# Optimization experiments

Measured on AMD Instinct MI355X. Metric: run time of the kernel, lower is better.

## Reference

```python
import jax, jax.numpy as jnp
import numpy as np

B, T, D, FF, H, K = 8, 1024, 512, 2048, 8, 15
HD = D // H  # key_dim = d_model // num_heads


def _ln(x, g, b):
    # keras LayerNormalization default epsilon = 1e-3
    m = jnp.mean(x, axis=-1, keepdims=True)
    v = jnp.var(x, axis=-1, keepdims=True)
    return (x - m) * jax.lax.rsqrt(v + 1e-3) * g + b


def setup_inputs() -> dict:
    key = jax.random.key(0)
    ks = iter(jax.random.split(key, 64))

    def rn(shape, s=0.02):
        return jax.random.normal(next(ks), shape, jnp.float32) * s

    p = {}
    p['x'] = jax.random.normal(next(ks), (B, T, D), jnp.float32)
    # ff_pre: LN -> Dense(FF, relu) -> Dense(D)
    p['g1'] = jnp.ones((D,), jnp.float32); p['b1'] = jnp.zeros((D,), jnp.float32)
    p['Wff1'] = rn((D, FF)); p['bff1'] = jnp.zeros((FF,), jnp.float32)
    p['Wff2'] = rn((FF, D)); p['bff2'] = jnp.zeros((D,), jnp.float32)
    # attention norm + MHA projections (keras EinsumDense shapes)
    p['ga'] = jnp.ones((D,), jnp.float32); p['ba'] = jnp.zeros((D,), jnp.float32)
    p['Wq'] = rn((D, H, HD)); p['bq'] = jnp.zeros((H, HD), jnp.float32)
    p['Wk'] = rn((D, H, HD)); p['bk'] = jnp.zeros((H, HD), jnp.float32)
    p['Wv'] = rn((D, H, HD)); p['bv'] = jnp.zeros((H, HD), jnp.float32)
    p['Wo'] = rn((H, HD, D)); p['bo'] = jnp.zeros((D,), jnp.float32)
    # conv branch: LN -> pointwise conv (2D, gelu) -> depthwise conv(k=15) -> BN -> swish -> pointwise conv (D)
    p['gc'] = jnp.ones((D,), jnp.float32); p['bc'] = jnp.zeros((D,), jnp.float32)
    p['Wcp'] = rn((D, 2 * D)); p['bcp'] = jnp.zeros((2 * D,), jnp.float32)
    p['dwk'] = rn((K, 1, 2 * D)); p['dwb'] = jnp.zeros((2 * D,), jnp.float32)
    p['bn_g'] = jnp.ones((2 * D,), jnp.float32); p['bn_b'] = jnp.zeros((2 * D,), jnp.float32)
    p['bn_m'] = jnp.zeros((2 * D,), jnp.float32)
    p['bn_v'] = jnp.ones((2 * D,), jnp.float32)
    p['Wco'] = rn((2 * D, D)); p['bco'] = jnp.zeros((D,), jnp.float32)
    # ff_post
    p['g2'] = jnp.ones((D,), jnp.float32); p['b2'] = jnp.zeros((D,), jnp.float32)
    p['Wf1'] = rn((D, FF)); p['bf1'] = jnp.zeros((FF,), jnp.float32)
    p['Wf2'] = rn((FF, D)); p['bf2'] = jnp.zeros((D,), jnp.float32)
    return p


def reference(x, g1, b1, Wff1, bff1, Wff2, bff2, ga, ba, Wq, bq, Wk, bk, Wv, bv, Wo, bo, gc, bc, Wcp, bcp, dwk, dwb, bn_g, bn_b, bn_m, bn_v, Wco, bco, g2, b2, Wf1, bf1, Wf2, bf2):
    # Macaron FFN (pre), half-step residual applied later
    x_ff = jnp.maximum(_ln(x, g1, b1) @ Wff1 + bff1, 0.0) @ Wff2 + bff2

    # causal multi-head self-attention (cache=None path)
    a = _ln(x, ga, ba)
    q = jnp.einsum('btd,dhk->bthk', a, Wq) + bq
    k = jnp.einsum('btd,dhk->bthk', a, Wk) + bk
    v = jnp.einsum('btd,dhk->bthk', a, Wv) + bv
    scores = jnp.einsum('bqhd,bkhd->bhqk', q, k) / jnp.sqrt(jnp.float32(HD))
    causal = jnp.tril(jnp.ones((T, T), bool))  # [T,T]
    scores = jnp.where(causal, scores, jnp.float32(-1e9))
    w = jax.nn.softmax(scores, axis=-1)
    ctx = jnp.einsum('bhqk,bkhd->bqhd', w, v)
    attn = jnp.einsum('bqhd,hdo->bqo', ctx, Wo) + bo

    x = x + 0.5 * x_ff + attn

    # convolution module: pointwise(gelu) -> causal left-pad -> depthwise -> BN(inference) -> swish -> pointwise
    c = jax.nn.gelu(_ln(x, gc, bc) @ Wcp + bcp, approximate=False)
    c = jnp.pad(c, ((0, 0), (K - 1, 0), (0, 0)))  # causal pad
    c = jax.lax.conv_general_dilated(
        c, dwk, window_strides=(1,), padding='VALID',
        dimension_numbers=('NWC', 'WIO', 'NWC'), feature_group_count=2 * D) + dwb
    c = (c - bn_m) * jax.lax.rsqrt(bn_v + 1e-3) * bn_g + bn_b
    c = c * jax.nn.sigmoid(c)  # swish
    c = c @ Wco + bco
    x = x + c

    # post FFN (full residual)
    x = x + (jnp.maximum(_ln(x, g2, b2) @ Wf1 + bf1, 0.0) @ Wf2 + bf2)
    return x
```

## Files before the change

### kernel.cpp

```cpp
#include <hip/hip_runtime.h>
#include <hip/hip_bf16.h>
#include <math.h>

#define BB 8
#define TT 1024
#define DD 512
#define FFD 2048
#define HH 8
#define HDD 64
#define KW 15
#define MR (BB*TT)
#define QKVN 1536

typedef __attribute__((ext_vector_type(8))) short short8;
typedef __attribute__((ext_vector_type(4))) short short4v;
typedef __attribute__((ext_vector_type(4))) float f32x4;
typedef __hip_bfloat16 bf16;

__device__ __forceinline__ float bf2f(unsigned u16) {
    return __uint_as_float(u16 << 16);
}

__device__ __forceinline__ void async_copy16(const void* g, void* l) {
    __builtin_amdgcn_global_load_lds(
        (const __attribute__((address_space(1))) void*)g,
        (__attribute__((address_space(3))) void*)l, 16, 0, 0);
}

__device__ __forceinline__ float gelu_exact(float v) {
    return 0.5f * v * (1.0f + erff(v * 0.70710678118654752f));
}

struct PrepPack {
    const float* src[10];
    bf16*        dst[10];
    int          K[10];
    int          lgNT[10];
    float        scale[10];
    int          off[10];
    const float* bq; const float* bk; const float* bv;
    float*       bdst;
    const float* x;
    const float* g1; const float* b1; const float* ga; const float* ba;
    bf16* o1; bf16* o2;
};

__global__ __launch_bounds__(256) void prep_kernel(PrepPack P) {
    __shared__ alignas(16) bf16 T[64][72];
    const int bid = blockIdx.x;
    if (bid == 1536) {
        #pragma unroll
        for (int it = 0; it < 6; ++it) {
            int i = it * 256 + threadIdx.x;
            float v = i < 512 ? P.bq[i] * 0.125f
                              : (i < 1024 ? P.bk[i - 512] : P.bv[i - 1024]);
            P.bdst[i] = v;
        }
        return;
    }
    if (bid > 1536) {
        int wave = ((bid - 1537) * 256 + (int)threadIdx.x) >> 6;
        int lane = threadIdx.x & 63;
        const float* row = P.x + (size_t)wave * DD;
        float4 v0 = ((const float4*)row)[lane];
        float4 v1 = ((const float4*)row)[64 + lane];
        float s  = v0.x + v0.y + v0.z + v0.w + v1.x + v1.y + v1.z + v1.w;
        float ss = v0.x*v0.x + v0.y*v0.y + v0.z*v0.z + v0.w*v0.w
                 + v1.x*v1.x + v1.y*v1.y + v1.z*v1.z + v1.w*v1.w;
        #pragma unroll
        for (int off = 32; off >= 1; off >>= 1) {
            s  += __shfl_xor(s,  off, 64);
            ss += __shfl_xor(ss, off, 64);
        }
        float mean = s * (1.0f / DD);
        float var  = ss * (1.0f / DD) - mean * mean;
        float r    = rsqrtf(var + 1e-3f);
        float n0x = (v0.x - mean) * r, n0y = (v0.y - mean) * r,
              n0z = (v0.z - mean) * r, n0w = (v0.w - mean) * r;
        float n1x = (v1.x - mean) * r, n1y = (v1.y - mean) * r,
              n1z = (v1.z - mean) * r, n1w = (v1.w - mean) * r;
        {
            float4 g0 = ((const float4*)P.g1)[lane];
            float4 gg = ((const float4*)P.g1)[64 + lane];
            float4 b0 = ((const float4*)P.b1)[lane];
            float4 bb = ((const float4*)P.b1)[64 + lane];
            alignas(8) bf16 o0[4], o1[4];
            o0[0] = __float2bfloat16(n0x * g0.x + b0.x);
            o0[1] = __float2bfloat16(n0y * g0.y + b0.y);
            o0[2] = __float2bfloat16(n0z * g0.z + b0.z);
            o0[3] = __float2bfloat16(n0w * g0.w + b0.w);
            o1[0] = __float2bfloat16(n1x * gg.x + bb.x);
            o1[1] = __float2bfloat16(n1y * gg.y + bb.y);
            o1[2] = __float2bfloat16(n1z * gg.z + bb.z);
            o1[3] = __float2bfloat16(n1w * gg.w + bb.w);
            bf16* orow = P.o1 + (size_t)wave * DD;
            *(short4v*)(orow + lane * 4)       = *(const short4v*)o0;
            *(short4v*)(orow + 256 + lane * 4) = *(const short4v*)o1;
        }
        {
            float4 g0 = ((const float4*)P.ga)[lane];
            float4 gg = ((const float4*)P.ga)[64 + lane];
            float4 b0 = ((const float4*)P.ba)[lane];
            float4 bb = ((const float4*)P.ba)[64 + lane];
            alignas(8) bf16 o0[4], o1[4];
            o0[0] = __float2bfloat16(n0x * g0.x + b0.x);
            o0[1] = __float2bfloat16(n0y * g0.y + b0.y);
            o0[2] = __float2bfloat16(n0z * g0.z + b0.z);
            o0[3] = __float2bfloat16(n0w * g0.w + b0.w);
            o1[0] = __float2bfloat16(n1x * gg.x + bb.x);
            o1[1] = __float2bfloat16(n1y * gg.y + bb.y);
            o1[2] = __float2bfloat16(n1z * gg.z + bb.z);
            o1[3] = __float2bfloat16(n1w * gg.w + bb.w);
            bf16* orow = P.o2 + (size_t)wave * DD;
            *(short4v*)(orow + lane * 4)       = *(const short4v*)o0;
            *(short4v*)(orow + 256 + lane * 4) = *(const short4v*)o1;
        }
        return;
    }
    int e = 0;
    #pragma unroll
    for (int i = 1; i < 10; ++i) e = (bid >= P.off[i]) ? i : e;
    const float* W  = P.src[e];
    bf16*        Wt = P.dst[e];
    const int    K  = P.K[e];
    const int    lg = P.lgNT[e];
    const float  scale = P.scale[e];
    const int local = bid - P.off[e];
    const int bx = local & ((1 << lg) - 1);
    const int by = local >> lg;
    const int k0 = by * 64;
    const int n0 = bx * 64;
    const int N  = (1 << lg) * 64;
    const int tid = threadIdx.x;
    #pragma unroll
    for (int it = 0; it < 4; ++it) {
        int lin = it * 256 + tid;
        int kl  = lin >> 4;
        int nq  = (lin & 15) * 4;
        float4 v = *(const float4*)(W + (size_t)(k0 + kl) * N + n0 + nq);
        T[nq + 0][kl] = __float2bfloat16(v.x * scale);
        T[nq + 1][kl] = __float2bfloat16(v.y * scale);
        T[nq + 2][kl] = __float2bfloat16(v.z * scale);
        T[nq + 3][kl] = __float2bfloat16(v.w * scale);
    }
    __syncthreads();
    #pragma unroll
    for (int it = 0; it < 4; ++it) {
        int lin = it * 256 + tid;
        int nl  = lin >> 4;
        int kq  = (lin & 15) * 4;
        *(short4v*)(Wt + (size_t)(n0 + nl) * K + k0 + kq) = *(const short4v*)&T[nl][kq];
    }
}

__global__ __launch_bounds__(256) void ln_kernel(const float* __restrict__ x,
                                                 const float* __restrict__ g,
                                                 const float* __restrict__ b,
                                                 bf16* __restrict__ out) {
    int wave = (blockIdx.x * blockDim.x + threadIdx.x) >> 6;
    int lane = threadIdx.x & 63;
    if (wave >= MR) return;
    const float* row = x + (size_t)wave * DD;
    float4 v0 = ((const float4*)row)[lane];
    float4 v1 = ((const float4*)row)[64 + lane];
    float s  = v0.x + v0.y + v0.z + v0.w + v1.x + v1.y + v1.z + v1.w;
    float ss = v0.x*v0.x + v0.y*v0.y + v0.z*v0.z + v0.w*v0.w
             + v1.x*v1.x + v1.y*v1.y + v1.z*v1.z + v1.w*v1.w;
    #pragma unroll
    for (int off = 32; off >= 1; off >>= 1) {
        s  += __shfl_xor(s,  off, 64);
        ss += __shfl_xor(ss, off, 64);
    }
    float mean = s * (1.0f / DD);
    float var  = ss * (1.0f / DD) - mean * mean;
    float r    = rsqrtf(var + 1e-3f);
    float4 g0 = ((const float4*)g)[lane];
    float4 g1 = ((const float4*)g)[64 + lane];
    float4 b0 = ((const float4*)b)[lane];
    float4 b1 = ((const float4*)b)[64 + lane];
    alignas(8) bf16 o0[4], o1[4];
    o0[0] = __float2bfloat16((v0.x - mean) * r * g0.x + b0.x);
    o0[1] = __float2bfloat16((v0.y - mean) * r * g0.y + b0.y);
    o0[2] = __float2bfloat16((v0.z - mean) * r * g0.z + b0.z);
    o0[3] = __float2bfloat16((v0.w - mean) * r * g0.w + b0.w);
    o1[0] = __float2bfloat16((v1.x - mean) * r * g1.x + b1.x);
    o1[1] = __float2bfloat16((v1.y - mean) * r * g1.y + b1.y);
    o1[2] = __float2bfloat16((v1.z - mean) * r * g1.z + b1.z);
    o1[3] = __float2bfloat16((v1.w - mean) * r * g1.w + b1.w);
    bf16* orow = out + (size_t)wave * DD;
    *(short4v*)(orow + lane * 4)       = *(const short4v*)o0;
    *(short4v*)(orow + 256 + lane * 4) = *(const short4v*)o1;
}

template<int BN, int OP, int RESMODE, int OUTMODE>
__global__ __launch_bounds__(256) void bgemm_kernel(
    const bf16* __restrict__ A,
    const bf16* __restrict__ Bt,
    const float* __restrict__ bias,
    const float* __restrict__ res1,
    const bf16* __restrict__ res2,
    float s2, float oscale,
    void* __restrict__ Cout,
    int N, int Kd, int nxb)
{
    constexpr int NT = BN / 32;
    __shared__ alignas(16) bf16 As[128][64];
    __shared__ alignas(16) bf16 Bs[BN][64];
    const int tid  = threadIdx.x;
    const int w    = tid >> 6;
    const int lane = tid & 63;
    const int quad = lane >> 4;
    const int l16  = lane & 15;
    const int wm   = w >> 1, wn = w & 1;

    const int flat = blockIdx.x;
    const int c8   = flat & 7;
    const int j    = flat >> 3;
    const int jy   = j / nxb;
    const int m0   = (c8 * 8 + jy) * 128;
    const int n0   = (j - jy * nxb) * BN;

    const int srow = lane >> 3;
    const int scol = ((lane & 7) ^ srow) * 8;

    const bf16* Ap = A  + (size_t)(m0 + w * 32 + srow) * Kd + scol;
    const bf16* Bp = Bt + (size_t)(n0 + w * (BN / 4) + srow) * Kd + scol;

    f32x4 acc[4][NT] = {};

    for (int k0 = 0; k0 < Kd; k0 += 64) {
        #pragma unroll
        for (int i = 0; i < 4; ++i)
            async_copy16(Ap + (size_t)(i * 8) * Kd + k0, &As[w * 32 + i * 8][0]);
        #pragma unroll
        for (int i = 0; i < BN / 32; ++i)
            async_copy16(Bp + (size_t)(i * 8) * Kd + k0, &Bs[w * (BN / 4) + i * 8][0]);
        __syncthreads();
        #pragma unroll
        for (int ks = 0; ks < 2; ++ks) {
            short8 af[4], bfr[NT];
            #pragma unroll
            for (int mt = 0; mt < 4; ++mt) {
                const int row = wm * 64 + mt * 16 + l16;
                const int c   = ((ks * 4 + quad) ^ (row & 7)) * 16;
                af[mt] = *(const short8*)((const char*)&As[row][0] + c);
            }
            #pragma unroll
            for (int nt = 0; nt < NT; ++nt) {
                const int col = wn * (BN / 2) + nt * 16 + l16;
                const int c   = ((ks * 4 + quad) ^ (col & 7)) * 16;
                bfr[nt] = *(const short8*)((const char*)&Bs[col][0] + c);
            }
            #pragma unroll
            for (int mt = 0; mt < 4; ++mt)
                #pragma unroll
                for (int nt = 0; nt < NT; ++nt)
                    acc[mt][nt] = __builtin_amdgcn_mfma_f32_16x16x32_bf16(
                        af[mt], bfr[nt], acc[mt][nt], 0, 0, 0);
        }
        __syncthreads();
    }

    const int crow0 = m0 + wm * 64 + quad * 4;
    const int ccol0 = n0 + wn * (BN / 2) + l16;
    #pragma unroll
    for (int nt = 0; nt < NT; ++nt) {
        const int col = ccol0 + nt * 16;
        const float bv = bias[col];
        #pragma unroll
        for (int mt = 0; mt < 4; ++mt) {
            #pragma unroll
            for (int r = 0; r < 4; ++r) {
                const int row = crow0 + mt * 16 + r;
                const size_t off = (size_t)row * N + col;
                float o = acc[mt][nt][r] + bv;
                if (OP == 1)      o = fmaxf(o, 0.f);
                else if (OP == 2) o = gelu_exact(o);
                if (RESMODE >= 1) o += res1[off];
                if (RESMODE == 2) o += s2 * __bfloat162float(res2[off]);
                if (OUTMODE == 0) ((float*)Cout)[off] = o;
                else              ((bf16*)Cout)[off]  = __float2bfloat16(o * oscale);
            }
        }
    }
}

__global__ __launch_bounds__(512, 2) void gemm256_kernel(
    const bf16* __restrict__ Aff, const bf16* __restrict__ Btff,
    const float* __restrict__ biasff, bf16* __restrict__ outff,
    const bf16* __restrict__ Aqk, const bf16* __restrict__ Btqk,
    const float* __restrict__ biasqk, bf16* __restrict__ qkvb,
    bf16* __restrict__ Vtb, int nffblk)
{
    __shared__ alignas(16) char lds[131072];
    const int tid  = threadIdx.x;
    const int w    = tid >> 6;
    const int lane = tid & 63;
    const int quad = lane >> 4;
    const int l16  = lane & 15;
    const int wm   = w >> 2, wn = w & 3;

    const bool jobq = (int)blockIdx.x >= nffblk;
    const int  flat = jobq ? (int)blockIdx.x - nffblk : (int)blockIdx.x;
    const int  nxb  = jobq ? 6 : 8;
    const bf16* A   = jobq ? Aqk : Aff;
    const bf16* Bt  = jobq ? Btqk : Btff;
    const float* bias = jobq ? biasqk : biasff;

    const int c8 = flat & 7;
    const int j  = flat >> 3;
    const int jy = j / nxb;
    const int m0 = (c8 * 4 + jy) * 256;
    const int n0 = (j - jy * nxb) * 256;

    const bf16* ApS = A  + (size_t)(m0 + w * 32 + (lane >> 2)) * DD + (lane & 3) * 8;
    const bf16* BpS = Bt + (size_t)(n0 + w * 32 + (lane >> 2)) * DD + (lane & 3) * 8;
    char* ldsW = lds + w * 2048;

#define STAGE_A(kc, boff) do { \
        async_copy16(ApS + (kc),            ldsW + (boff));        \
        async_copy16(ApS + 16 * DD + (kc),  ldsW + (boff) + 1024); } while (0)
#define STAGE_B(kc, boff) do { \
        async_copy16(BpS + (kc),            ldsW + (boff));        \
        async_copy16(BpS + 16 * DD + (kc),  ldsW + (boff) + 1024); } while (0)

    const int aoff = (wm * 128 + l16) * 64 + quad * 16;
    const int boff = 32768 + (wn * 64 + l16) * 64 + quad * 16;

    f32x4 acc[8][4] = {};

#define CLUSTER(MH) \
    asm volatile("" ::: "memory"); \
    __builtin_amdgcn_s_barrier(); \
    asm volatile("s_waitcnt lgkmcnt(0)" ::: "memory"); \
    __builtin_amdgcn_sched_barrier(0); \
    __builtin_amdgcn_s_setprio(1); \
    _Pragma("unroll") \
    for (int mt = 0; mt < 4; ++mt) \
        _Pragma("unroll") \
        for (int nt = 0; nt < 4; ++nt) \
            acc[(MH) * 4 + mt][nt] = __builtin_amdgcn_mfma_f32_16x16x32_bf16( \
                af[mt], bf[nt], acc[(MH) * 4 + mt][nt], 0, 0, 0); \
    __builtin_amdgcn_s_setprio(0); \
    asm volatile("" ::: "memory"); \
    __builtin_amdgcn_s_barrier();

    STAGE_A(0,  0);      STAGE_B(0,  32768);
    STAGE_A(32, 16384);  STAGE_B(32, 49152);
    STAGE_A(64, 65536);  STAGE_B(64, 65536 + 32768);
    asm volatile("s_waitcnt vmcnt(4)" ::: "memory");
    __builtin_amdgcn_s_barrier();

    for (int t = 0; t < 8; ++t) {
        const int cb = (t & 1) * 65536;
        const int nb = cb ^ 65536;
        short8 af[4], bf[4];

        #pragma unroll
        for (int nt = 0; nt < 4; ++nt)
            bf[nt] = *(const short8*)(lds + cb + boff + nt * 1024);
        #pragma unroll
        for (int mt = 0; mt < 4; ++mt)
            af[mt] = *(const short8*)(lds + cb + aoff + mt * 1024);
        if (t < 7) STAGE_A((t + 1) * 64 + 32, nb + 16384);
        CLUSTER(0)

        #pragma unroll
        for (int mt = 0; mt < 4; ++mt)
            af[mt] = *(const short8*)(lds + cb + aoff + 4096 + mt * 1024);
        if (t < 7) STAGE_B((t + 1) * 64 + 32, nb + 49152);
        CLUSTER(1)

        #pragma unroll
        for (int nt = 0; nt < 4; ++nt)
            bf[nt] = *(const short8*)(lds + cb + 16384 + boff + nt * 1024);
        #pragma unroll
        for (int mt = 0; mt < 4; ++mt)
            af[mt] = *(const short8*)(lds + cb + 16384 + aoff + mt * 1024);
        if (t < 6) STAGE_A((t + 2) * 64, cb);
        CLUSTER(0)

        #pragma unroll
        for (int mt = 0; mt < 4; ++mt)
            af[mt] = *(const short8*)(lds + cb + 16384 + aoff + 4096 + mt * 1024);
        if (t < 6) STAGE_B((t + 2) * 64, cb + 32768);
        if (t < 6)       { asm volatile("s_waitcnt vmcnt(4)" ::: "memory"); }
        else if (t == 6) { asm volatile("s_waitcnt vmcnt(0)" ::: "memory"); }
        CLUSTER(1)
    }
#undef CLUSTER
#undef STAGE_A
#undef STAGE_B

    const int crow0 = m0 + wm * 128 + quad * 4;
    const int ccol0 = n0 + wn * 64 + l16;
    if (jobq) {
        #pragma unroll
        for (int nt = 0; nt < 4; ++nt) {
            const int col = ccol0 + nt * 16;
            const float bv = bias[col];
            #pragma unroll
            for (int mt = 0; mt < 8; ++mt) {
                alignas(8) bf16 o4[4];
                #pragma unroll
                for (int r = 0; r < 4; ++r)
                    o4[r] = __float2bfloat16(acc[mt][nt][r] + bv);
                const int rowt = crow0 + mt * 16;
                if (col < 1024) {
                    #pragma unroll
                    for (int r = 0; r < 4; ++r)
                        qkvb[(size_t)(rowt + r) * QKVN + col] = o4[r];
                } else {
                    const int dg  = col - 1024;
                    const int bb  = rowt >> 10, t0 = rowt & 1023;
                    const int bh2 = bb * 8 + (dg >> 6), d = dg & 63;
                    *(short4v*)(Vtb + ((size_t)bh2 * 64 + d) * TT + t0) =
                        *(const short4v*)o4;
                }
            }
        }
    } else {
        #pragma unroll
        for (int nt = 0; nt < 4; ++nt) {
            const int col = ccol0 + nt * 16;
            const float bv = bias[col];
            #pragma unroll
            for (int mt = 0; mt < 8; ++mt) {
                #pragma unroll
                for (int r = 0; r < 4; ++r) {
                    const float o = fmaxf(acc[mt][nt][r] + bv, 0.f);
                    outff[(size_t)(crow0 + mt * 16 + r) * FFD + col] =
                        __float2bfloat16(o);
                }
            }
        }
    }
}

__global__ __launch_bounds__(256) void ff2attn_kernel(
    const bf16* __restrict__ QKV, const bf16* __restrict__ Vt,
    bf16* __restrict__ ctx,
    const bf16* __restrict__ bigb, const bf16* __restrict__ Wff2t,
    const float* __restrict__ bff2, bf16* __restrict__ xffb)
{
    __shared__ alignas(16) bf16 smem[16384];
    const int tid  = threadIdx.x;
    const int w    = tid >> 6;
    const int lane = tid & 63;
    const int quad = lane >> 4;
    const int l16  = lane & 15;

    if (blockIdx.x < 512) {
        typedef bf16 (*tile_t)[64][64];
        tile_t Ks = (tile_t)smem;
        tile_t Vs = (tile_t)(smem + 2 * 64 * 64);
        const int bh = blockIdx.x & 63;
        const int bi = 7 - ((int)blockIdx.x >> 6);
        const int b = bh >> 3, h = bh & 7;

        const bf16* Qg = QKV + (size_t)(b * TT) * QKVN + h * 64;
        const bf16* Kg = QKV + (size_t)(b * TT) * QKVN + 512 + h * 64;
        const bf16* Vg = Vt  + (size_t)bh * 64 * TT;

        const int qL = bi * 128 + w * 16;
        const int qH = qL + 64;
        short8 qfL0 = *(const short8*)(Qg + (size_t)(qL + l16) * QKVN + quad * 8);
        short8 qfL1 = *(const short8*)(Qg + (size_t)(qL + l16) * QKVN + 32 + quad * 8);
        short8 qfH0 = *(const short8*)(Qg + (size_t)(qH + l16) * QKVN + quad * 8);
        short8 qfH1 = *(const short8*)(Qg + (size_t)(qH + l16) * QKVN + 32 + quad * 8);

        const int sgrow  = lane >> 3;
        const int sgchnk = lane & 7;

        f32x4 caccL[4] = {}, caccH[4] = {};
        float lL = 0.f, lH = 0.f;
        const int prow_base = ((l16 >> 2) << 3) + (l16 & 3);
        const int smax = 2 * bi + 1;

        #pragma unroll
        for (int i = 0; i < 2; ++i) {
            const int rowbase = w * 8 + i * 32;
            const int row = rowbase + sgrow;
            const int fR = (row & 3) | (((row >> 3) & 1) << 2);
            const int sc = sgchnk ^ fR;
            async_copy16(Kg + (size_t)row * QKVN + sc * 8, &Ks[0][rowbase][0]);
            async_copy16(Vg + (size_t)row * TT + sc * 8,   &Vs[0][rowbase][0]);
        }

        int buf = 0;
        for (int s = 0; s <= smax; ++s) {
            __syncthreads();
            if (s < smax) {
                const int kn = (s + 1) * 64;
                #pragma unroll
                for (int i = 0; i < 2; ++i) {
                    const int rowbase = w * 8 + i * 32;
                    const int row = rowbase + sgrow;
                    const int fR = (row & 3) | (((row >> 3) & 1) << 2);
                    const int sc = sgchnk ^ fR;
                    async_copy16(Kg + (size_t)(kn + row) * QKVN + sc * 8,
                                 &Ks[buf ^ 1][rowbase][0]);
                    async_copy16(Vg + (size_t)row * TT + kn + sc * 8,
                                 &Vs[buf ^ 1][rowbase][0]);
                }
            }
            const int k0 = s * 64;
            const bool doL = (s < smax);

            f32x4 sTL[4], sTH[4];
            #pragma unroll
            for (int s4 = 0; s4 < 4; ++s4) {
                const int prow = prow_base + (s4 >> 1) * 32 + (s4 & 1) * 4;
                const int fR = (prow & 3) | (((prow >> 3) & 1) << 2);
                short8 ka = *(const short8*)&Ks[buf][prow][(quad ^ fR) * 8];
                short8 kb = *(const short8*)&Ks[buf][prow][((4 + quad) ^ fR) * 8];
                f32x4 zH = {0.f, 0.f, 0.f, 0.f};
                zH = __builtin_amdgcn_mfma_f32_16x16x32_bf16(ka, qfH0, zH, 0, 0, 0);
                sTH[s4] = __builtin_amdgcn_mfma_f32_16x16x32_bf16(kb, qfH1, zH, 0, 0, 0);
                if (doL) {
                    f32x4 zL = {0.f, 0.f, 0.f, 0.f};
                    zL = __builtin_amdgcn_mfma_f32_16x16x32_bf16(ka, qfL0, zL, 0, 0, 0);
                    sTL[s4] = __builtin_amdgcn_mfma_f32_16x16x32_bf16(kb, qfL1, zL, 0, 0, 0);
                }
            }

            alignas(16) bf16 pbH[16], pbL[16];
            if (s == smax) {
                const int qg = qH + l16;
                #pragma unroll
                for (int s4 = 0; s4 < 4; ++s4)
                    #pragma unroll
                    for (int r = 0; r < 4; ++r) {
                        const int key = k0 + (s4 >> 1) * 32 + quad * 8 + (s4 & 1) * 4 + r;
                        const float p = (key <= qg) ? __expf(sTH[s4][r]) : 0.f;
                        lH += p;
                        pbH[s4 * 4 + r] = __float2bfloat16(p);
                    }
            } else {
                #pragma unroll
                for (int s4 = 0; s4 < 4; ++s4)
                    #pragma unroll
                    for (int r = 0; r < 4; ++r) {
                        const float p = __expf(sTH[s4][r]);
                        lH += p;
                        pbH[s4 * 4 + r] = __float2bfloat16(p);
                    }
            }
            if (doL) {
                if (s == smax - 1) {
                    const int qg = qL + l16;
                    #pragma unroll
                    for (int s4 = 0; s4 < 4; ++s4)
                        #pragma unroll
                        for (int r = 0; r < 4; ++r) {
                            const int key = k0 + (s4 >> 1) * 32 + quad * 8 + (s4 & 1) * 4 + r;
                            const float p = (key <= qg) ? __expf(sTL[s4][r]) : 0.f;
                            lL += p;
                            pbL[s4 * 4 + r] = __float2bfloat16(p);
                        }
                } else {
                    #pragma unroll
                    for (int s4 = 0; s4 < 4; ++s4)
                        #pragma unroll
                        for (int r = 0; r < 4; ++r) {
                            const float p = __expf(sTL[s4][r]);
                            lL += p;
                            pbL[s4 * 4 + r] = __float2bfloat16(p);
                        }
                }
            }
            const short8 pfH0 = *(const short8*)&pbH[0];
            const short8 pfH1 = *(const short8*)&pbH[8];
            const short8 pfL0 = *(const short8*)&pbL[0];
            const short8 pfL1 = *(const short8*)&pbL[8];

            #pragma unroll
            for (int g = 0; g < 4; ++g) {
                const int vrow = g * 16 + l16;
                const int fR = (vrow & 3) | (((vrow >> 3) & 1) << 2);
                short8 va = *(const short8*)&Vs[buf][vrow][(quad ^ fR) * 8];
                short8 vb = *(const short8*)&Vs[buf][vrow][((4 + quad) ^ fR) * 8];
                caccH[g] = __builtin_amdgcn_mfma_f32_16x16x32_bf16(va, pfH0, caccH[g], 0, 0, 0);
                caccH[g] = __builtin_amdgcn_mfma_f32_16x16x32_bf16(vb, pfH1, caccH[g], 0, 0, 0);
                if (doL) {
                    caccL[g] = __builtin_amdgcn_mfma_f32_16x16x32_bf16(va, pfL0, caccL[g], 0, 0, 0);
                    caccL[g] = __builtin_amdgcn_mfma_f32_16x16x32_bf16(vb, pfL1, caccL[g], 0, 0, 0);
                }
            }
            buf ^= 1;
        }

        lL += __shfl_xor(lL, 16, 64);
        lL += __shfl_xor(lL, 32, 64);
        lH += __shfl_xor(lH, 16, 64);
        lH += __shfl_xor(lH, 32, 64);
        const float invL = 1.0f / lL;
        const float invH = 1.0f / lH;

        bf16* CbL = ctx + (size_t)(b * TT + qL + l16) * DD + h * 64;
        bf16* CbH = ctx + (size_t)(b * TT + qH + l16) * DD + h * 64;
        #pragma unroll
        for (int g = 0; g < 4; ++g) {
            alignas(8) bf16 oL[4], oH[4];
            #pragma unroll
            for (int r = 0; r < 4; ++r) {
                oL[r] = __float2bfloat16(caccL[g][r] * invL);
                oH[r] = __float2bfloat16(caccH[g][r] * invH);
            }
            *(short4v*)(CbL + g * 16 + quad * 4) = *(const short4v*)oL;
            *(short4v*)(CbH + g * 16 + quad * 4) = *(const short4v*)oH;
        }
    } else {
        typedef bf16 (*row_t)[64];
        row_t As = (row_t)smem;
        row_t Bs = (row_t)(smem + 128 * 64);
        const int wm = w >> 1, wn = w & 1;

        const int flat = (int)blockIdx.x - 512;
        const int c8 = flat & 7;
        const int j  = flat >> 3;
        const int jy = j >> 3;
        const int m0 = (c8 * 8 + jy) * 128;
        const int n0 = (j & 7) * 64;

        const int srow = lane >> 3;
        const int scol = ((lane & 7) ^ srow) * 8;

        const bf16* Ap = bigb  + (size_t)(m0 + w * 32 + srow) * FFD + scol;
        const bf16* Bp = Wff2t + (size_t)(n0 + w * 16 + srow) * FFD + scol;

        f32x4 acc[4][2] = {};

        for (int k0 = 0; k0 < FFD; k0 += 64) {
            #pragma unroll
            for (int i = 0; i < 4; ++i)
                async_copy16(Ap + (size_t)(i * 8) * FFD + k0, &As[w * 32 + i * 8][0]);
            #pragma unroll
            for (int i = 0; i < 2; ++i)
                async_copy16(Bp + (size_t)(i * 8) * FFD + k0, &Bs[w * 16 + i * 8][0]);
            __syncthreads();
            #pragma unroll
            for (int ks = 0; ks < 2; ++ks) {
                short8 af[4], bfr[2];
                #pragma unroll
                for (int mt = 0; mt < 4; ++mt) {
                    const int row = wm * 64 + mt * 16 + l16;
                    const int c   = ((ks * 4 + quad) ^ (row & 7)) * 16;
                    af[mt] = *(const short8*)((const char*)&As[row][0] + c);
                }
                #pragma unroll
                for (int nt = 0; nt < 2; ++nt) {
                    const int col = wn * 32 + nt * 16 + l16;
                    const int c   = ((ks * 4 + quad) ^ (col & 7)) * 16;
                    bfr[nt] = *(const short8*)((const char*)&Bs[col][0] + c);
                }
                #pragma unroll
                for (int mt = 0; mt < 4; ++mt)
                    #pragma unroll
                    for (int nt = 0; nt < 2; ++nt)
                        acc[mt][nt] = __builtin_amdgcn_mfma_f32_16x16x32_bf16(
                            af[mt], bfr[nt], acc[mt][nt], 0, 0, 0);
            }
            __syncthreads();
        }

        const int crow0 = m0 + wm * 64 + quad * 4;
        const int ccol0 = n0 + wn * 32 + l16;
        #pragma unroll
        for (int nt = 0; nt < 2; ++nt) {
            const int col = ccol0 + nt * 16;
            const float bv = bff2[col];
            #pragma unroll
            for (int mt = 0; mt < 4; ++mt)
                #pragma unroll
                for (int r = 0; r < 4; ++r) {
                    const int row = crow0 + mt * 16 + r;
                    xffb[(size_t)row * DD + col] =
                        __float2bfloat16(acc[mt][nt][r] + bv);
                }
        }
    }
}

__global__ __launch_bounds__(256) void dwconv_kernel(const bf16* __restrict__ c1,
                                                     const float* __restrict__ dwk,
                                                     const float* __restrict__ dwb,
                                                     const float* __restrict__ bn_g,
                                                     const float* __restrict__ bn_b,
                                                     const float* __restrict__ bn_m,
                                                     const float* __restrict__ bn_v,
                                                     bf16* __restrict__ out) {
    const int C2 = 2 * DD;
    const int lin = blockIdx.x * 256 + threadIdx.x;
    const int chp = lin & 511;
    const int ch  = chp << 1;
    const int tch = lin >> 9;
    const int row0 = tch << 4;
    const int t0   = row0 & (TT - 1);

    float w0[KW], w1[KW];
    #pragma unroll
    for (int i = 0; i < KW; ++i) {
        w0[i] = dwk[i * C2 + ch];
        w1[i] = dwk[i * C2 + ch + 1];
    }
    const float a0 = rsqrtf(bn_v[ch] + 1e-3f) * bn_g[ch];
    const float a1 = rsqrtf(bn_v[ch + 1] + 1e-3f) * bn_g[ch + 1];
    const float c0 = (dwb[ch] - bn_m[ch]) * a0 + bn_b[ch];
    const float c1v = (dwb[ch + 1] - bn_m[ch + 1]) * a1 + bn_b[ch + 1];

    float x0[30], x1[30];
    if (t0 >= KW - 1) {
        #pragma unroll
        for (int i = 0; i < 30; ++i) {
            unsigned u = *(const unsigned*)(c1 + (size_t)(row0 - (KW - 1) + i) * C2 + ch);
            x0[i] = bf2f(u & 0xffff);
            x1[i] = bf2f(u >> 16);
        }
    } else {
        #pragma unroll
        for (int i = 0; i < 30; ++i) {
            unsigned u = 0;
            if (t0 - (KW - 1) + i >= 0)
                u = *(const unsigned*)(c1 + (size_t)(row0 - (KW - 1) + i) * C2 + ch);
            x0[i] = bf2f(u & 0xffff);
            x1[i] = bf2f(u >> 16);
        }
    }

    #pragma unroll
    for (int j = 0; j < 16; ++j) {
        float s0 = 0.f, s1 = 0.f;
        #pragma unroll
        for (int i = 0; i < KW; ++i) {
            s0 += x0[j + i] * w0[i];
            s1 += x1[j + i] * w1[i];
        }
        s0 = s0 * a0 + c0;
        s1 = s1 * a1 + c1v;
        s0 = s0 / (1.f + __expf(-s0));
        s1 = s1 / (1.f + __expf(-s1));
        alignas(4) bf16 ob[2] = {__float2bfloat16(s0), __float2bfloat16(s1)};
        *(unsigned*)(out + (size_t)(row0 + j) * C2 + ch) = *(const unsigned*)ob;
    }
}

extern "C" void kernel_launch(void* const* d_in, const int* in_sizes, int n_in,
                              void* d_out, int out_size, void* d_ws, size_t ws_size,
                              hipStream_t stream) {
    const float* x    = (const float*)d_in[0];
    const float* g1   = (const float*)d_in[1];
    const float* b1   = (const float*)d_in[2];
    const float* Wff1 = (const float*)d_in[3];
    const float* bff1 = (const float*)d_in[4];
    const float* Wff2 = (const float*)d_in[5];
    const float* bff2 = (const float*)d_in[6];
    const float* ga   = (const float*)d_in[7];
    const float* ba   = (const float*)d_in[8];
    const float* Wq   = (const float*)d_in[9];
    const float* bq   = (const float*)d_in[10];
    const float* Wk   = (const float*)d_in[11];
    const float* bk   = (const float*)d_in[12];
    const float* Wv   = (const float*)d_in[13];
    const float* bv   = (const float*)d_in[14];
    const float* Wo   = (const float*)d_in[15];
    const float* bo   = (const float*)d_in[16];
    const float* gc   = (const float*)d_in[17];
    const float* bc   = (const float*)d_in[18];
    const float* Wcp  = (const float*)d_in[19];
    const float* bcp  = (const float*)d_in[20];
    const float* dwk  = (const float*)d_in[21];
    const float* dwb  = (const float*)d_in[22];
    const float* bn_g = (const float*)d_in[23];
    const float* bn_b = (const float*)d_in[24];
    const float* bn_m = (const float*)d_in[25];
    const float* bn_v = (const float*)d_in[26];
    const float* Wco  = (const float*)d_in[27];
    const float* bco  = (const float*)d_in[28];
    const float* g2   = (const float*)d_in[29];
    const float* b2   = (const float*)d_in[30];
    const float* Wf1  = (const float*)d_in[31];
    const float* bf1  = (const float*)d_in[32];
    const float* Wf2  = (const float*)d_in[33];
    const float* bf2  = (const float*)d_in[34];

    float* out = (float*)d_out;

    char* p = (char*)d_ws;
    bf16* lnb   = (bf16*)p;  p += (size_t)MR * DD * 2;
    bf16* lnab  = (bf16*)p;  p += (size_t)MR * DD * 2;
    bf16* qkvb  = (bf16*)p;  p += (size_t)MR * QKVN * 2;
    bf16* Vtb   = (bf16*)p;  p += (size_t)MR * DD * 2;
    bf16* ctxb  = (bf16*)p;  p += (size_t)MR * DD * 2;
    bf16* xffb  = (bf16*)p;  p += (size_t)MR * DD * 2;
    bf16* bigb  = (bf16*)p;  p += (size_t)MR * FFD * 2;
    bf16* c2b   = (bf16*)p;  p += (size_t)MR * 1024 * 2;
    bf16* Wff1t = (bf16*)p;  p += (size_t)FFD * DD * 2;
    bf16* Wff2t = (bf16*)p;  p += (size_t)DD * FFD * 2;
    bf16* Wqkvt = (bf16*)p;  p += (size_t)QKVN * DD * 2;
    bf16* Wot   = (bf16*)p;  p += (size_t)DD * DD * 2;
    bf16* Wcpt  = (bf16*)p;  p += (size_t)1024 * DD * 2;
    bf16* Wcot  = (bf16*)p;  p += (size_t)DD * 1024 * 2;
    bf16* Wf1t  = (bf16*)p;  p += (size_t)FFD * DD * 2;
    bf16* Wf2t  = (bf16*)p;  p += (size_t)DD * FFD * 2;
    float* bqkv = (float*)p; p += QKVN * 4;

    dim3 blk(256);

    PrepPack P;
    auto set = [&](int i, const float* s, bf16* d, int K, int N, float sc, int off) {
        P.src[i] = s; P.dst[i] = d; P.K[i] = K; P.scale[i] = sc; P.off[i] = off;
        int nt = N / 64, lg = 0; while ((1 << lg) < nt) ++lg; P.lgNT[i] = lg;
    };
    set(0, Wff1, Wff1t, DD,  FFD, 1.f,    0);
    set(1, Wff2, Wff2t, FFD, DD,  1.f,    256);
    set(2, Wq,   Wqkvt,                DD, DD, 0.125f, 512);
    set(3, Wk,   Wqkvt + (size_t)512 * DD,  DD, DD, 1.f, 576);
    set(4, Wv,   Wqkvt + (size_t)1024 * DD, DD, DD, 1.f, 640);
    set(5, Wo,   Wot,   DD,  DD,  1.f,    704);
    set(6, Wcp,  Wcpt,  DD,  1024, 1.f,   768);
    set(7, Wco,  Wcot,  1024, DD, 1.f,    896);
    set(8, Wf1,  Wf1t,  DD,  FFD, 1.f,    1024);
    set(9, Wf2,  Wf2t,  FFD, DD,  1.f,    1280);
    P.bq = bq; P.bk = bk; P.bv = bv; P.bdst = bqkv;
    P.x = x; P.g1 = g1; P.b1 = b1; P.ga = ga; P.ba = ba;
    P.o1 = lnb; P.o2 = lnab;

    prep_kernel<<<dim3(1537 + MR / 4), blk, 0, stream>>>(P);
    gemm256_kernel<<<dim3(448), dim3(512), 0, stream>>>(
        lnb, Wff1t, bff1, bigb, lnab, Wqkvt, bqkv, qkvb, Vtb, 256);
    ff2attn_kernel<<<dim3(1024), blk, 0, stream>>>(
        qkvb, Vtb, ctxb, bigb, Wff2t, bff2, xffb);
    bgemm_kernel<64, 0, 2, 0><<<dim3(8 * 64), blk, 0, stream>>>(
        ctxb, Wot, bo, x, xffb, 0.5f, 1.f, out, DD, DD, 8);
    ln_kernel<<<dim3(MR / 4), blk, 0, stream>>>(out, gc, bc, lnb);
    bgemm_kernel<128, 2, 0, 1><<<dim3(8 * 64), blk, 0, stream>>>(
        lnb, Wcpt, bcp, nullptr, nullptr, 0.f, 1.f, bigb, 1024, DD, 8);
    dwconv_kernel<<<dim3(MR * 512 / 16 / 256), blk, 0, stream>>>(
        bigb, dwk, dwb, bn_g, bn_b, bn_m, bn_v, c2b);
    bgemm_kernel<64, 0, 1, 0><<<dim3(8 * 64), blk, 0, stream>>>(
        c2b, Wcot, bco, out, nullptr, 0.f, 1.f, out, DD, 1024, 8);
    ln_kernel<<<dim3(MR / 4), blk, 0, stream>>>(out, g2, b2, lnb);
    gemm256_kernel<<<dim3(256), dim3(512), 0, stream>>>(
        lnb, Wf1t, bf1, bigb, nullptr, nullptr, nullptr, nullptr, nullptr, 256);
    bgemm_kernel<64, 0, 1, 0><<<dim3(8 * 64), blk, 0, stream>>>(
        bigb, Wf2t, bf2, out, nullptr, 0.f, 1.f, out, DD, FFD, 8);
}
```

Baseline: 374.7 us.

## Double-buffer LDS tiles in GEMM loops and interleave attention/FF2 blocks

Both the generic bf16 GEMM and the FF2 branch of the fused attention kernel now use two LDS buffers. The next K tile is prefetched with async global-to-LDS copies while the current one is consumed, synchronised by explicit vmcnt waits and raw barriers plus setprio around the MFMA section. The fused kernel also alternates attention and FF2 blocks by block-index parity instead of running them in two contiguous ranges, to balance the mix on each CU. The cost is more LDS per block, which may lower occupancy, and hand-counted vmcnt values that must match the number of outstanding copies.

New measurement: 367.0 us. -2.0%, faster.

```diff
diff --git a/kernel.cpp b/kernel.cpp
--- a/kernel.cpp
+++ b/kernel.cpp
@@ -204,8 +204,9 @@
     int N, int Kd, int nxb)
 {
     constexpr int NT = BN / 32;
-    __shared__ alignas(16) bf16 As[128][64];
-    __shared__ alignas(16) bf16 Bs[BN][64];
+    constexpr int S  = 4 + BN / 32;
+    __shared__ alignas(16) bf16 As[2][128][64];
+    __shared__ alignas(16) bf16 Bs[2][BN][64];
     const int tid  = threadIdx.x;
     const int w    = tid >> 6;
     const int lane = tid & 63;
@@ -227,15 +228,30 @@
     const bf16* Bp = Bt + (size_t)(n0 + w * (BN / 4) + srow) * Kd + scol;
 
     f32x4 acc[4][NT] = {};
-
-    for (int k0 = 0; k0 < Kd; k0 += 64) {
-        #pragma unroll
-        for (int i = 0; i < 4; ++i)
-            async_copy16(Ap + (size_t)(i * 8) * Kd + k0, &As[w * 32 + i * 8][0]);
-        #pragma unroll
-        for (int i = 0; i < BN / 32; ++i)
-            async_copy16(Bp + (size_t)(i * 8) * Kd + k0, &Bs[w * (BN / 4) + i * 8][0]);
-        __syncthreads();
+    const int nk = Kd >> 6;
+
+#define BSTAGE(bb, kk) do { \
+        _Pragma("unroll") \
+        for (int i = 0; i < 4; ++i) \
+            async_copy16(Ap + (size_t)(i * 8) * Kd + (kk), &As[bb][w * 32 + i * 8][0]); \
+        _Pragma("unroll") \
+        for (int i = 0; i < BN / 32; ++i) \
+            async_copy16(Bp + (size_t)(i * 8) * Kd + (kk), &Bs[bb][w * (BN / 4) + i * 8][0]); \
+    } while (0)
+
+    BSTAGE(0, 0);
+    for (int t = 0; t < nk; ++t) {
+        const int cur = t & 1;
+        if (t + 1 < nk) {
+            BSTAGE(cur ^ 1, (t + 1) * 64);
+            if constexpr (S == 6) asm volatile("s_waitcnt vmcnt(6)" ::: "memory");
+            else                  asm volatile("s_waitcnt vmcnt(8)" ::: "memory");
+        } else {
+            asm volatile("s_waitcnt vmcnt(0)" ::: "memory");
+        }
+        __builtin_amdgcn_s_barrier();
+        __builtin_amdgcn_sched_barrier(0);
+        __builtin_amdgcn_s_setprio(1);
         #pragma unroll
         for (int ks = 0; ks < 2; ++ks) {
             short8 af[4], bfr[NT];
@@ -243,13 +259,13 @@
             for (int mt = 0; mt < 4; ++mt) {
                 const int row = wm * 64 + mt * 16 + l16;
                 const int c   = ((ks * 4 + quad) ^ (row & 7)) * 16;
-                af[mt] = *(const short8*)((const char*)&As[row][0] + c);
+                af[mt] = *(const short8*)((const char*)&As[cur][row][0] + c);
             }
             #pragma unroll
             for (int nt = 0; nt < NT; ++nt) {
                 const int col = wn * (BN / 2) + nt * 16 + l16;
                 const int c   = ((ks * 4 + quad) ^ (col & 7)) * 16;
-                bfr[nt] = *(const short8*)((const char*)&Bs[col][0] + c);
+                bfr[nt] = *(const short8*)((const char*)&Bs[cur][col][0] + c);
             }
             #pragma unroll
             for (int mt = 0; mt < 4; ++mt)
@@ -258,8 +274,11 @@
                     acc[mt][nt] = __builtin_amdgcn_mfma_f32_16x16x32_bf16(
                         af[mt], bfr[nt], acc[mt][nt], 0, 0, 0);
         }
-        __syncthreads();
-    }
+        __builtin_amdgcn_s_setprio(0);
+        asm volatile("" ::: "memory");
+        __builtin_amdgcn_s_barrier();
+    }
+#undef BSTAGE
 
     const int crow0 = m0 + wm * 64 + quad * 4;
     const int ccol0 = n0 + wn * (BN / 2) + l16;
@@ -443,19 +462,20 @@
     const bf16* __restrict__ bigb, const bf16* __restrict__ Wff2t,
     const float* __restrict__ bff2, bf16* __restrict__ xffb)
 {
-    __shared__ alignas(16) bf16 smem[16384];
+    __shared__ alignas(16) bf16 smem[24576];
     const int tid  = threadIdx.x;
     const int w    = tid >> 6;
     const int lane = tid & 63;
     const int quad = lane >> 4;
     const int l16  = lane & 15;
-
-    if (blockIdx.x < 512) {
+    const int half = (int)blockIdx.x >> 1;
+
+    if ((blockIdx.x & 1) == 0) {
         typedef bf16 (*tile_t)[64][64];
         tile_t Ks = (tile_t)smem;
         tile_t Vs = (tile_t)(smem + 2 * 64 * 64);
-        const int bh = blockIdx.x & 63;
-        const int bi = 7 - ((int)blockIdx.x >> 6);
+        const int bh = half & 63;
+        const int bi = 7 - (half >> 6);
         const int b = bh >> 3, h = bh & 7;
 
         const bf16* Qg = QKV + (size_t)(b * TT) * QKVN + h * 64;
@@ -611,12 +631,9 @@
             *(short4v*)(CbH + g * 16 + quad * 4) = *(const short4v*)oH;
         }
     } else {
-        typedef bf16 (*row_t)[64];
-        row_t As = (row_t)smem;
-        row_t Bs = (row_t)(smem + 128 * 64);
         const int wm = w >> 1, wn = w & 1;
 
-        const int flat = (int)blockIdx.x - 512;
+        const int flat = half;
         const int c8 = flat & 7;
         const int j  = flat >> 3;
         const int jy = j >> 3;
@@ -631,14 +648,31 @@
 
         f32x4 acc[4][2] = {};
 
-        for (int k0 = 0; k0 < FFD; k0 += 64) {
-            #pragma unroll
-            for (int i = 0; i < 4; ++i)
-                async_copy16(Ap + (size_t)(i * 8) * FFD + k0, &As[w * 32 + i * 8][0]);
-            #pragma unroll
-            for (int i = 0; i < 2; ++i)
-                async_copy16(Bp + (size_t)(i * 8) * FFD + k0, &Bs[w * 16 + i * 8][0]);
-            __syncthreads();
+#define FSTAGE(bb, kk) do { \
+        _Pragma("unroll") \
+        for (int i = 0; i < 4; ++i) \
+            async_copy16(Ap + (size_t)(i * 8) * FFD + (kk), \
+                         smem + (bb) * 8192 + (w * 32 + i * 8) * 64); \
+        _Pragma("unroll") \
+        for (int i = 0; i < 2; ++i) \
+            async_copy16(Bp + (size_t)(i * 8) * FFD + (kk), \
+                         smem + 16384 + (bb) * 4096 + (w * 16 + i * 8) * 64); \
+    } while (0)
+
+        FSTAGE(0, 0);
+        for (int t = 0; t < 32; ++t) {
+            const int cur = t & 1;
+            if (t < 31) {
+                FSTAGE(cur ^ 1, (t + 1) * 64);
+                asm volatile("s_waitcnt vmcnt(6)" ::: "memory");
+            } else {
+                asm volatile("s_waitcnt vmcnt(0)" ::: "memory");
+            }
+            __builtin_amdgcn_s_barrier();
+            __builtin_amdgcn_sched_barrier(0);
+            const bf16* AsB = smem + cur * 8192;
+            const bf16* BsB = smem + 16384 + cur * 4096;
+            __builtin_amdgcn_s_setprio(1);
             #pragma unroll
             for (int ks = 0; ks < 2; ++ks) {
                 short8 af[4], bfr[2];
@@ -646,13 +680,13 @@
                 for (int mt = 0; mt < 4; ++mt) {
                     const int row = wm * 64 + mt * 16 + l16;
                     const int c   = ((ks * 4 + quad) ^ (row & 7)) * 16;
-                    af[mt] = *(const short8*)((const char*)&As[row][0] + c);
+                    af[mt] = *(const short8*)((const char*)(AsB + row * 64) + c);
                 }
                 #pragma unroll
                 for (int nt = 0; nt < 2; ++nt) {
                     const int col = wn * 32 + nt * 16 + l16;
                     const int c   = ((ks * 4 + quad) ^ (col & 7)) * 16;
-                    bfr[nt] = *(const short8*)((const char*)&Bs[col][0] + c);
+                    bfr[nt] = *(const short8*)((const char*)(BsB + col * 64) + c);
                 }
                 #pragma unroll
                 for (int mt = 0; mt < 4; ++mt)
@@ -661,8 +695,11 @@
                         acc[mt][nt] = __builtin_amdgcn_mfma_f32_16x16x32_bf16(
                             af[mt], bfr[nt], acc[mt][nt], 0, 0, 0);
             }
-            __syncthreads();
-        }
+            __builtin_amdgcn_s_setprio(0);
+            asm volatile("" ::: "memory");
+            __builtin_amdgcn_s_barrier();
+        }
+#undef FSTAGE
 
         const int crow0 = m0 + wm * 64 + quad * 4;
         const int ccol0 = n0 + wn * 32 + l16;
```
